# Kernel optimization log

Measured on AMD Instinct MI355X. Metric: run time of the kernel, lower is better.

Reference implementation:

```python
import jax, jax.numpy as jnp
import numpy as np

B, L, CIN, DLOI, NPTS0, NPTS1, H = 2, 5000, 256, 128, 32, 8, 256
HALF = DLOI // 2
EPS = 1e-5


def _bn_params(k, c):
    k1, k2, k3, k4 = jax.random.split(k, 4)
    gamma = 1.0 + 0.1 * jax.random.normal(k1, (c,), jnp.float32)
    beta = 0.1 * jax.random.normal(k2, (c,), jnp.float32)
    mean = 0.1 * jax.random.normal(k3, (c,), jnp.float32)
    var = 0.5 + jax.random.uniform(k4, (c,), jnp.float32)
    return jnp.stack([gamma, beta, mean, var])  # [4, c]


def setup_inputs():
    key = jax.random.key(0)
    ks = jax.random.split(key, 12)
    feature = jax.random.normal(ks[0], (B, CIN, H, H), jnp.float32)
    lines = jax.random.uniform(ks[1], (B, L, 2, 2), jnp.float32, minval=0.0, maxval=255.0)
    w_fc1 = 0.05 * jax.random.normal(ks[2], (DLOI, CIN), jnp.float32)
    b_fc1 = jnp.zeros((DLOI,), jnp.float32)
    bn1 = _bn_params(ks[3], DLOI)
    c1_w = 0.1 * jax.random.normal(ks[4], (HALF, DLOI), jnp.float32)
    c1_b = jnp.zeros((HALF,), jnp.float32)
    bn2 = _bn_params(ks[5], HALF)
    c2_w = 0.1 * jax.random.normal(ks[6], (HALF, HALF, 3), jnp.float32)
    c2_b = jnp.zeros((HALF,), jnp.float32)
    bn3 = _bn_params(ks[7], HALF)
    c3_w = 0.1 * jax.random.normal(ks[8], (DLOI, HALF), jnp.float32)
    c3_b = jnp.zeros((DLOI,), jnp.float32)
    w_fc2 = 0.03 * jax.random.normal(ks[9], (4, DLOI * NPTS1), jnp.float32)
    b_fc2 = jnp.zeros((4,), jnp.float32)
    return {"feature": feature, "lines": lines, "w_fc1": w_fc1, "b_fc1": b_fc1,
            "bn1": bn1, "c1_w": c1_w, "c1_b": c1_b, "bn2": bn2, "c2_w": c2_w,
            "c2_b": c2_b, "bn3": bn3, "c3_w": c3_w, "c3_b": c3_b,
            "w_fc2": w_fc2, "b_fc2": b_fc2}


def _bn(v, p):
    # v: [N, C, P], p: [4, C] = gamma, beta, running_mean, running_var (eval mode)
    scale = (p[0] * jax.lax.rsqrt(p[3] + EPS))[None, :, None]
    shift = p[1][None, :, None]
    return (v - p[2][None, :, None]) * scale + shift


def _forward(feature, lines, w_fc1, b_fc1, bn1, c1_w, c1_b, bn2, c2_w, c2_b,
             bn3, c3_w, c3_b, w_fc2, b_fc2):
    # fc1: 1x1 conv over backbone feature -> [B, DLOI, H, H]
    x = jnp.einsum('bchw,oc->bohw', feature, w_fc1) + b_fc1[None, :, None, None]

    # sample NPTS0 points along each line: p = p0*lam + p1*(1-lam) - 0.5
    lam = jnp.linspace(0.0, 1.0, NPTS0, dtype=jnp.float32)[:, None]  # [NPTS0, 1]
    p = lines[:, :, 0:1, :] * lam + lines[:, :, 1:2, :] * (1.0 - lam) - 0.5  # [B,L,NPTS0,2]
    px, py = p[..., 0], p[..., 1]
    px0 = jnp.clip(jnp.floor(px), 0.0, H - 1.0)
    py0 = jnp.clip(jnp.floor(py), 0.0, H - 1.0)
    px1 = jnp.clip(px0 + 1.0, 0.0, H - 1.0)
    py1 = jnp.clip(py0 + 1.0, 0.0, H - 1.0)
    i0, j0 = px0.astype(jnp.int32), py0.astype(jnp.int32)
    i1, j1 = px1.astype(jnp.int32), py1.astype(jnp.int32)
    w00 = (px1 - px) * (py1 - py)
    w10 = (px - px0) * (py1 - py)
    w01 = (px1 - px) * (py - py0)
    w11 = (px - px0) * (py - py0)

    def gather_one(feat, i0b, j0b, i1b, j1b, a, b, c, d):
        # feat [C,H,W]; indices/weights [L, NPTS0] -> [C, L, NPTS0]
        return (feat[:, i0b, j0b] * a + feat[:, i1b, j0b] * b
                + feat[:, i0b, j1b] * c + feat[:, i1b, j1b] * d)

    xp = jax.vmap(gather_one)(x, i0, j0, i1, j1, w00, w10, w01, w11)  # [B,C,L,NPTS0]
    xp = xp.transpose(0, 2, 1, 3).reshape(B * L, DLOI, NPTS0)

    # MaxPool1d(kernel=4, stride=4): NPTS0 -> NPTS1
    xp = xp.reshape(B * L, DLOI, NPTS1, NPTS0 // NPTS1).max(-1)

    # Bottleneck1D (eval-mode BN): x + op(x)
    h = jax.nn.relu(_bn(xp, bn1))
    h = jnp.einsum('ncp,oc->nop', h, c1_w) + c1_b[None, :, None]
    h = jax.nn.relu(_bn(h, bn2))
    h = jax.lax.conv_general_dilated(h, c2_w, window_strides=(1,), padding=((1, 1),),
                                     dimension_numbers=('NCH', 'OIH', 'NCH')) + c2_b[None, :, None]
    h = jax.nn.relu(_bn(h, bn3))
    h = jnp.einsum('ncp,oc->nop', h, c3_w) + c3_b[None, :, None]
    y = xp + h

    # fc2: ReLU + Linear(DLOI*NPTS1 -> 4), then softmax scores
    flat = y.reshape(B * L, DLOI * NPTS1)
    logits = jax.nn.relu(flat) @ w_fc2.T + b_fc2
    s = jax.nn.softmax(logits, axis=-1)
    return s


def reference(feature, lines, w_fc1, b_fc1, bn1, c1_w, c1_b, bn2, c2_w, c2_b,
              bn3, c3_w, c3_b, w_fc2, b_fc2):
    return _forward(feature, lines, w_fc1, b_fc1, bn1, c1_w, c1_b, bn2, c2_w,
                    c2_b, bn3, c3_w, c3_b, w_fc2, b_fc2)
```

## Files before the change

### kernel.cpp

```cpp
#include <hip/hip_runtime.h>
#include <math.h>
#include <stdint.h>

#define HH 256
#define HW 65536
#define CIN 256
#define DLOI 128
#define NLINES 10000
#define LPB 5000

typedef _Float16 h2v  __attribute__((ext_vector_type(2)));
typedef _Float16 f16x8 __attribute__((ext_vector_type(8)));
typedef float    f32x4 __attribute__((ext_vector_type(4)));

__device__ __forceinline__ h2v u2h(unsigned int u) { return __builtin_bit_cast(h2v, u); }
__device__ __forceinline__ unsigned int h2u(h2v h) { return __builtin_bit_cast(unsigned int, h); }

__device__ __forceinline__ float fdot2(h2v a, unsigned int w, float c) {
#if __has_builtin(__builtin_amdgcn_fdot2)
    return __builtin_amdgcn_fdot2(a, u2h(w), c, false);
#else
    h2v b = u2h(w);
    return c + (float)a[0] * (float)b[0] + (float)a[1] * (float)b[1];
#endif
}

__device__ __forceinline__ h2v relu2(h2v a) {
    h2v z = (h2v)(_Float16)0.f;
#if __has_builtin(__builtin_elementwise_max)
    return __builtin_elementwise_max(a, z);
#else
    h2v r; r[0] = a[0] > z[0] ? a[0] : z[0]; r[1] = a[1] > z[1] ? a[1] : z[1]; return r;
#endif
}
__device__ __forceinline__ h2v hmax2v(h2v a, h2v b) {
#if __has_builtin(__builtin_elementwise_max)
    return __builtin_elementwise_max(a, b);
#else
    h2v r; r[0] = a[0] > b[0] ? a[0] : b[0]; r[1] = a[1] > b[1] ? a[1] : b[1]; return r;
#endif
}

__global__ __launch_bounds__(256) void prep_small(
    const float* __restrict__ w_fc1, const float* __restrict__ c1w,
    const float* __restrict__ c2w,  const float* __restrict__ c3w,
    const float* __restrict__ wfc2, const float* __restrict__ bn1,
    const float* __restrict__ bn2,  const float* __restrict__ bn3,
    _Float16* __restrict__ wf16, unsigned int* __restrict__ c1w16,
    unsigned int* __restrict__ c2w16, unsigned int* __restrict__ c3w16,
    unsigned int* __restrict__ wfc2p, unsigned int* __restrict__ bn_pk)
{
    int i = blockIdx.x * 256 + threadIdx.x;
    if (i < 32768) { wf16[i] = (_Float16)w_fc1[i]; return; }
    i -= 32768;
    if (i < 4096) {
        int c2 = i >> 6, o = i & 63;
        h2v v = { (_Float16)c1w[o * 128 + 2 * c2], (_Float16)c1w[o * 128 + 2 * c2 + 1] };
        c1w16[c2 * 64 + o] = h2u(v); return;
    }
    i -= 4096;
    if (i < 6144) {
        int o = i & 63, rem = i >> 6; int tap = rem % 3, i2 = rem / 3;
        h2v v = { (_Float16)c2w[(o * 64 + 2 * i2) * 3 + tap],
                  (_Float16)c2w[(o * 64 + 2 * i2 + 1) * 3 + tap] };
        c2w16[(i2 * 3 + tap) * 64 + o] = h2u(v); return;
    }
    i -= 6144;
    if (i < 4096) {
        int o = i & 127, i2 = i >> 7;
        h2v v = { (_Float16)c3w[o * 64 + 2 * i2], (_Float16)c3w[o * 64 + 2 * i2 + 1] };
        c3w16[i2 * 128 + o] = h2u(v); return;
    }
    i -= 4096;
    if (i < 2048) {
        int c2 = i & 63, p = (i >> 6) & 7, j = i >> 9;
        h2v v = { (_Float16)wfc2[j * 1024 + (2 * c2) * 8 + p],
                  (_Float16)wfc2[j * 1024 + (2 * c2 + 1) * 8 + p] };
        wfc2p[(j * 8 + p) * 64 + c2] = h2u(v); return;
    }
    i -= 2048;
    if (i < 128) {
        const float* bn; int C, base, hcount;
        if (i < 64)      { bn = bn1; C = 128; base = 0;   hcount = 64; }
        else if (i < 96) { bn = bn2; C = 64;  base = 128; hcount = 32; i -= 64; }
        else             { bn = bn3; C = 64;  base = 192; hcount = 32; i -= 96; }
        int c0 = 2 * i, c1 = 2 * i + 1;
        float s0 = bn[c0] * rsqrtf(bn[3 * C + c0] + 1e-5f);
        float s1 = bn[c1] * rsqrtf(bn[3 * C + c1] + 1e-5f);
        float h0 = bn[C + c0] - bn[2 * C + c0] * s0;
        float h1 = bn[C + c1] - bn[2 * C + c1] * s1;
        h2v sv = { (_Float16)s0, (_Float16)s1 };
        h2v hv = { (_Float16)h0, (_Float16)h1 };
        bn_pk[base + i] = h2u(sv);
        bn_pk[base + hcount + i] = h2u(hv);
    }
}

__global__ __launch_bounds__(256, 4) void fc1_fused(
    const float* __restrict__ feat,
    const _Float16* __restrict__ W,
    const float* __restrict__ bias,
    unsigned int* __restrict__ X)
{
    __shared__ float Tf[32 * 132];
    __shared__ _Float16 Wl[128 * 40];
    const int t = threadIdx.x;
    const int lane = t & 63, wave = t >> 6;
    const int wm = wave & 1, wn = wave >> 1;
    const int pix0g = blockIdx.x << 7;
    const int b = blockIdx.x >> 9;
    const int pix0l = pix0g & 65535;
    const float* fbase = feat + (size_t)b * (256u * 65536u) + pix0l;

    f32x4 acc[4][4];
#pragma unroll
    for (int a = 0; a < 4; a++)
#pragma unroll
        for (int c = 0; c < 4; c++) acc[a][c] = (f32x4)0.f;

    for (int ks = 0; ks < 8; ks++) {
        const int k0 = ks * 32;
        __syncthreads();
#pragma unroll
        for (int r = 0; r < 4; r++) {
            int idx = t + r * 256;
            int c = idx >> 5, p4 = idx & 31;
            float4 v = *(const float4*)(fbase + (size_t)(k0 + c) * 65536 + p4 * 4);
            *(float4*)&Tf[c * 132 + p4 * 4] = v;
        }
#pragma unroll
        for (int r = 0; r < 2; r++) {
            int idx = t + r * 256;
            int row = idx >> 2, ko = (idx & 3) * 8;
            *(uint4*)&Wl[row * 40 + ko] = *(const uint4*)(W + row * 256 + k0 + ko);
        }
        __syncthreads();
        f16x8 af[4], bf[4];
#pragma unroll
        for (int mt = 0; mt < 4; mt++)
            af[mt] = *(const f16x8*)&Wl[(wm * 64 + mt * 16 + (lane & 15)) * 40 + (lane >> 4) * 8];
#pragma unroll
        for (int nt = 0; nt < 4; nt++) {
            int q = wn * 64 + nt * 16 + (lane & 15);
            int cb = (lane >> 4) * 8;
            f16x8 v;
#pragma unroll
            for (int j = 0; j < 8; j++) v[j] = (_Float16)Tf[(cb + j) * 132 + q];
            bf[nt] = v;
        }
#pragma unroll
        for (int mt = 0; mt < 4; mt++)
#pragma unroll
            for (int nt = 0; nt < 4; nt++)
                acc[mt][nt] = __builtin_amdgcn_mfma_f32_16x16x32_f16(af[mt], bf[nt], acc[mt][nt], 0, 0, 0);
    }
#pragma unroll
    for (int mt = 0; mt < 4; mt++) {
        int o = wm * 64 + mt * 16 + (lane >> 4) * 4;
        float4 b4 = *(const float4*)(bias + o);
#pragma unroll
        for (int nt = 0; nt < 4; nt++) {
            int pix = pix0g + wn * 64 + nt * 16 + (lane & 15);
            f32x4 a = acc[mt][nt];
            h2v lo = { (_Float16)(a[0] + b4.x), (_Float16)(a[1] + b4.y) };
            h2v hi = { (_Float16)(a[2] + b4.z), (_Float16)(a[3] + b4.w) };
            uint2 v = { h2u(lo), h2u(hi) };
            *(uint2*)(X + (size_t)pix * 64 + (o >> 1)) = v;
        }
    }
}

__global__ __launch_bounds__(256, 4) void line_v3(
    const unsigned int* __restrict__ X,
    const float* __restrict__ lines,
    const unsigned int* __restrict__ c1w16, const float* __restrict__ c1b,
    const unsigned int* __restrict__ c2w16, const float* __restrict__ c2b,
    const unsigned int* __restrict__ c3w16, const float* __restrict__ c3b,
    const unsigned int* __restrict__ wfc2p, const float* __restrict__ bfc2,
    const unsigned int* __restrict__ bn_pk,
    float* __restrict__ out)
{
    __shared__ int geoB[256];
    __shared__ unsigned int geoWA[256], geoWB[256];
    __shared__ h2v xp[64 * 65];
    __shared__ h2v hb[32 * 65];
    __shared__ h2v ap[32 * 73];
    __shared__ float red[128];

    const int t = threadIdx.x;
    const int n0 = blockIdx.x * 8;
    const int col = t & 63;
    const int og = t >> 6;

    {
        int l = t >> 5, k = t & 31;
        int n = n0 + l;
        float4 ln = *(const float4*)(lines + n * 4);
        float lam = (float)k / 31.0f;
        float px = ln.x * lam + ln.z * (1.f - lam) - 0.5f;
        float py = ln.y * lam + ln.w * (1.f - lam) - 0.5f;
        float px0 = fminf(fmaxf(floorf(px), 0.f), 255.f);
        float py0 = fminf(fmaxf(floorf(py), 0.f), 255.f);
        float dx = px - px0, dy = py - py0;
        float ex = 1.f - dx, ey = 1.f - dy;
        h2v wA = { (_Float16)(ex * ey), (_Float16)(dx * ey) };
        h2v wB = { (_Float16)(ex * dy), (_Float16)(dx * dy) };
        int b = (n >= LPB) ? 1 : 0;
        int pixflat = (b << 16) + ((int)px0 << 8) + (int)py0;
        geoB[t] = pixflat << 6;
        geoWA[t] = h2u(wA); geoWB[t] = h2u(wB);
    }
    __syncthreads();

    {
        const int c8 = t & 15;
        const int sub = t >> 4;
        const int line = sub >> 1;
        const int gbase = (sub & 1) * 4;
        const uint4* xq = (const uint4*)X;
#pragma unroll
        for (int lg = 0; lg < 4; lg++) {
            int g = gbase + lg;
            int ptb = line * 32 + g * 4;
            h2v m0, m1, m2, m3;
#pragma unroll
            for (int s = 0; s < 4; s++) {
                int pt = ptb + s;
                int base4 = (geoB[pt] >> 2) + c8;
                h2v wA = u2h(geoWA[pt]), wB = u2h(geoWB[pt]);
                uint4 q00 = xq[base4];
                uint4 q10 = xq[base4 + 4096];
                uint4 q01 = xq[base4 + 16];
                uint4 q11 = xq[base4 + 4112];
                h2v w00 = { wA[0], wA[0] }, w10 = { wA[1], wA[1] };
                h2v w01 = { wB[0], wB[0] }, w11 = { wB[1], wB[1] };
                h2v v0 = u2h(q00.x) * w00 + u2h(q10.x) * w10 + u2h(q01.x) * w01 + u2h(q11.x) * w11;
                h2v v1 = u2h(q00.y) * w00 + u2h(q10.y) * w10 + u2h(q01.y) * w01 + u2h(q11.y) * w11;
                h2v v2 = u2h(q00.z) * w00 + u2h(q10.z) * w10 + u2h(q01.z) * w01 + u2h(q11.z) * w11;
                h2v v3 = u2h(q00.w) * w00 + u2h(q10.w) * w10 + u2h(q01.w) * w01 + u2h(q11.w) * w11;
                if (s == 0) { m0 = v0; m1 = v1; m2 = v2; m3 = v3; }
                else { m0 = hmax2v(m0, v0); m1 = hmax2v(m1, v1);
                       m2 = hmax2v(m2, v2); m3 = hmax2v(m3, v3); }
            }
            int colw = line * 8 + g;
            xp[(c8 * 4 + 0) * 65 + colw] = m0;
            xp[(c8 * 4 + 1) * 65 + colw] = m1;
            xp[(c8 * 4 + 2) * 65 + colw] = m2;
            xp[(c8 * 4 + 3) * 65 + colw] = m3;
        }
    }
    __syncthreads();

    {
        const int obU = __builtin_amdgcn_readfirstlane(og * 16);
        float acc[16];
#pragma unroll
        for (int i = 0; i < 16; i++) acc[i] = c1b[obU + i];
#pragma unroll 8
        for (int c2 = 0; c2 < 64; c2++) {
            h2v sc = u2h(bn_pk[c2]), sh = u2h(bn_pk[64 + c2]);
            h2v av = relu2(xp[c2 * 65 + col] * sc + sh);
            unsigned int wv[16];
#pragma unroll
            for (int q = 0; q < 4; q++)
                *(uint4*)&wv[q * 4] = *(const uint4*)(c1w16 + c2 * 64 + obU + q * 4);
#pragma unroll
            for (int i = 0; i < 16; i++) acc[i] = fdot2(av, wv[i], acc[i]);
        }
#pragma unroll
        for (int j = 0; j < 8; j++) {
            h2v v = { (_Float16)acc[2 * j], (_Float16)acc[2 * j + 1] };
            hb[(obU / 2 + j) * 65 + col] = v;
        }
    }
    __syncthreads();

    {
        int c2 = t >> 3, l = t & 7;
        h2v sc = u2h(bn_pk[128 + c2]), sh = u2h(bn_pk[160 + c2]);
        h2v z = (h2v)(_Float16)0.f;
        ap[c2 * 73 + l * 9] = z;
#pragma unroll
        for (int p = 0; p < 8; p++)
            ap[c2 * 73 + l * 9 + 1 + p] = relu2(hb[c2 * 65 + l * 8 + p] * sc + sh);
        if (l == 7) ap[c2 * 73 + 72] = z;
    }
    __syncthreads();

    {
        const int obU = __builtin_amdgcn_readfirstlane(og * 16);
        const int l = col >> 3, p = col & 7;
        const int pos0 = l * 9 + p;
        float acc[16];
#pragma unroll
        for (int i = 0; i < 16; i++) acc[i] = c2b[obU + i];
#pragma unroll 2
        for (int i2 = 0; i2 < 32; i2++) {
            h2v a0 = ap[i2 * 73 + pos0];
            h2v a1 = ap[i2 * 73 + pos0 + 1];
            h2v a2 = ap[i2 * 73 + pos0 + 2];
            unsigned int wv[48];
#pragma unroll
            for (int tap = 0; tap < 3; tap++)
#pragma unroll
                for (int q = 0; q < 4; q++)
                    *(uint4*)&wv[tap * 16 + q * 4] =
                        *(const uint4*)(c2w16 + (i2 * 3 + tap) * 64 + obU + q * 4);
#pragma unroll
            for (int i = 0; i < 16; i++) {
                acc[i] = fdot2(a0, wv[i], acc[i]);
                acc[i] = fdot2(a1, wv[16 + i], acc[i]);
                acc[i] = fdot2(a2, wv[32 + i], acc[i]);
            }
        }
#pragma unroll
        for (int j = 0; j < 8; j++) {
            h2v v = { (_Float16)acc[2 * j], (_Float16)acc[2 * j + 1] };
            hb[(obU / 2 + j) * 65 + col] = v;
        }
    }
    __syncthreads();

#pragma unroll
    for (int r = 0; r < 8; r++) {
        int idx = t + 256 * r;
        int c2 = idx >> 6, cl = idx & 63;
        h2v sc = u2h(bn_pk[192 + c2]), sh = u2h(bn_pk[224 + c2]);
        ap[c2 * 64 + cl] = relu2(hb[c2 * 65 + cl] * sc + sh);
    }
    __syncthreads();

    {
        const int obU = __builtin_amdgcn_readfirstlane(og * 32);
        float acc[32];
#pragma unroll
        for (int i = 0; i < 32; i++) acc[i] = c3b[obU + i];
#pragma unroll 2
        for (int i2 = 0; i2 < 32; i2++) {
            h2v av = ap[i2 * 64 + col];
            unsigned int wv[32];
#pragma unroll
            for (int q = 0; q < 8; q++)
                *(uint4*)&wv[q * 4] = *(const uint4*)(c3w16 + i2 * 128 + obU + q * 4);
#pragma unroll
            for (int i = 0; i < 32; i++) acc[i] = fdot2(av, wv[i], acc[i]);
        }
        const int p = col & 7, l = col >> 3;
        h2v yv[16];
#pragma unroll
        for (int j = 0; j < 16; j++) {
            h2v hv = { (_Float16)acc[2 * j], (_Float16)acc[2 * j + 1] };
            yv[j] = relu2(xp[(obU / 2 + j) * 65 + col] + hv);
        }
        float aj[4] = { 0.f, 0.f, 0.f, 0.f };
#pragma unroll
        for (int j = 0; j < 4; j++) {
            unsigned int wv2[16];
#pragma unroll
            for (int q = 0; q < 4; q++)
                *(uint4*)&wv2[q * 4] = *(const uint4*)(wfc2p + (j * 8 + p) * 64 + obU / 2 + q * 4);
#pragma unroll
            for (int j16 = 0; j16 < 16; j16++) aj[j] = fdot2(yv[j16], wv2[j16], aj[j]);
        }
#pragma unroll
        for (int off = 4; off > 0; off >>= 1) {
#pragma unroll
            for (int j = 0; j < 4; j++) aj[j] += __shfl_down(aj[j], off, 8);
        }
        if ((t & 7) == 0) {
#pragma unroll
            for (int j = 0; j < 4; j++) red[og * 32 + l * 4 + j] = aj[j];
        }
    }
    __syncthreads();

    if (t < 8) {
        float lg[4];
#pragma unroll
        for (int j = 0; j < 4; j++)
            lg[j] = bfc2[j] + red[t * 4 + j] + red[32 + t * 4 + j]
                  + red[64 + t * 4 + j] + red[96 + t * 4 + j];
        float mx = fmaxf(fmaxf(lg[0], lg[1]), fmaxf(lg[2], lg[3]));
        float e0 = expf(lg[0] - mx), e1 = expf(lg[1] - mx);
        float e2 = expf(lg[2] - mx), e3 = expf(lg[3] - mx);
        float s = 1.f / (e0 + e1 + e2 + e3);
        float4 r = { e0 * s, e1 * s, e2 * s, e3 * s };
        *(float4*)(out + (size_t)(n0 + t) * 4) = r;
    }
}

extern "C" void kernel_launch(void* const* d_in, const int* in_sizes, int n_in,
                              void* d_out, int out_size, void* d_ws, size_t ws_size,
                              hipStream_t stream) {
    const float* feature = (const float*)d_in[0];
    const float* lines   = (const float*)d_in[1];
    const float* w_fc1   = (const float*)d_in[2];
    const float* b_fc1   = (const float*)d_in[3];
    const float* bn1     = (const float*)d_in[4];
    const float* c1_w    = (const float*)d_in[5];
    const float* c1_b    = (const float*)d_in[6];
    const float* bn2     = (const float*)d_in[7];
    const float* c2_w    = (const float*)d_in[8];
    const float* c2_b    = (const float*)d_in[9];
    const float* bn3     = (const float*)d_in[10];
    const float* c3_w    = (const float*)d_in[11];
    const float* c3_b    = (const float*)d_in[12];
    const float* w_fc2   = (const float*)d_in[13];
    const float* b_fc2   = (const float*)d_in[14];
    float* out = (float*)d_out;

    char* ws = (char*)d_ws;
    unsigned int* X     = (unsigned int*)ws;
    _Float16*     wf16  = (_Float16*)(ws + 33554432);
    unsigned int* c1w16 = (unsigned int*)(ws + 33619968);
    unsigned int* c2w16 = (unsigned int*)(ws + 33636352);
    unsigned int* c3w16 = (unsigned int*)(ws + 33660928);
    unsigned int* wfc2p = (unsigned int*)(ws + 33677312);
    unsigned int* bn_pk = (unsigned int*)(ws + 33685504);

    prep_small<<<193, 256, 0, stream>>>(w_fc1, c1_w, c2_w, c3_w, w_fc2, bn1, bn2, bn3,
                                        wf16, c1w16, c2w16, c3w16, wfc2p, bn_pk);
    fc1_fused<<<1024, 256, 0, stream>>>(feature, wf16, b_fc1, X);
    line_v3<<<1250, 256, 0, stream>>>(X, lines, c1w16, c1_b, c2w16, c2_b,
                                      c3w16, c3_b, wfc2p, b_fc2, bn_pk, out);
}
```

Baseline: 318.9 us.

## Move bottleneck convolutions in line kernel from fdot2 to MFMA

Rewrites the three per-line bottleneck layers (1x1, 3-tap, 1x1 convs) to use 16x16x32 f16 MFMA instructions instead of scalar packed fdot2 loops. Weights are re-laid out row-major in f16 for MFMA A-fragments, and activations are stored in LDS in a column-major padded layout. BN1 and ReLU are fused into the sampling/maxpool stage, and the residual add is applied in the MFMA epilogue. The aim is to cut the VALU-bound dot-product work. In exchange there are more LDS layout constraints, an extra buffer, and padding-zero handling for the conv taps.

```diff
diff --git a/kernel.cpp b/kernel.cpp
--- a/kernel.cpp
+++ b/kernel.cpp
@@ -3,10 +3,6 @@
 #include <stdint.h>
 
 #define HH 256
-#define HW 65536
-#define CIN 256
-#define DLOI 128
-#define NLINES 10000
 #define LPB 5000
 
 typedef _Float16 h2v  __attribute__((ext_vector_type(2)));
@@ -46,32 +42,26 @@
     const float* __restrict__ c2w,  const float* __restrict__ c3w,
     const float* __restrict__ wfc2, const float* __restrict__ bn1,
     const float* __restrict__ bn2,  const float* __restrict__ bn3,
-    _Float16* __restrict__ wf16, unsigned int* __restrict__ c1w16,
-    unsigned int* __restrict__ c2w16, unsigned int* __restrict__ c3w16,
+    _Float16* __restrict__ wf16, _Float16* __restrict__ w1r,
+    _Float16* __restrict__ w2r, _Float16* __restrict__ w3r,
     unsigned int* __restrict__ wfc2p, unsigned int* __restrict__ bn_pk)
 {
     int i = blockIdx.x * 256 + threadIdx.x;
     if (i < 32768) { wf16[i] = (_Float16)w_fc1[i]; return; }
     i -= 32768;
-    if (i < 4096) {
-        int c2 = i >> 6, o = i & 63;
-        h2v v = { (_Float16)c1w[o * 128 + 2 * c2], (_Float16)c1w[o * 128 + 2 * c2 + 1] };
-        c1w16[c2 * 64 + o] = h2u(v); return;
-    }
-    i -= 4096;
-    if (i < 6144) {
-        int o = i & 63, rem = i >> 6; int tap = rem % 3, i2 = rem / 3;
-        h2v v = { (_Float16)c2w[(o * 64 + 2 * i2) * 3 + tap],
-                  (_Float16)c2w[(o * 64 + 2 * i2 + 1) * 3 + tap] };
-        c2w16[(i2 * 3 + tap) * 64 + o] = h2u(v); return;
-    }
-    i -= 6144;
-    if (i < 4096) {
-        int o = i & 127, i2 = i >> 7;
-        h2v v = { (_Float16)c3w[o * 64 + 2 * i2], (_Float16)c3w[o * 64 + 2 * i2 + 1] };
-        c3w16[i2 * 128 + o] = h2u(v); return;
-    }
-    i -= 4096;
+    if (i < 8192) {
+        w1r[i] = (_Float16)c1w[i]; return;
+    }
+    i -= 8192;
+    if (i < 12288) {
+        int ii = i & 63, o = (i >> 6) & 63, tap = i >> 12;
+        w2r[i] = (_Float16)c2w[(o * 64 + ii) * 3 + tap]; return;
+    }
+    i -= 12288;
+    if (i < 8192) {
+        w3r[i] = (_Float16)c3w[i]; return;
+    }
+    i -= 8192;
     if (i < 2048) {
         int c2 = i & 63, p = (i >> 6) & 7, j = i >> 9;
         h2v v = { (_Float16)wfc2[j * 1024 + (2 * c2) * 8 + p],
@@ -170,27 +160,29 @@
     }
 }
 
-__global__ __launch_bounds__(256, 4) void line_v3(
+__global__ __launch_bounds__(256, 4) void line_v4(
     const unsigned int* __restrict__ X,
     const float* __restrict__ lines,
-    const unsigned int* __restrict__ c1w16, const float* __restrict__ c1b,
-    const unsigned int* __restrict__ c2w16, const float* __restrict__ c2b,
-    const unsigned int* __restrict__ c3w16, const float* __restrict__ c3b,
+    const _Float16* __restrict__ w1r, const float* __restrict__ c1b,
+    const _Float16* __restrict__ w2r, const float* __restrict__ c2b,
+    const _Float16* __restrict__ w3r, const float* __restrict__ c3b,
     const unsigned int* __restrict__ wfc2p, const float* __restrict__ bfc2,
     const unsigned int* __restrict__ bn_pk,
     float* __restrict__ out)
 {
     __shared__ int geoB[256];
     __shared__ unsigned int geoWA[256], geoWB[256];
-    __shared__ h2v xp[64 * 65];
-    __shared__ h2v hb[32 * 65];
-    __shared__ h2v ap[32 * 73];
+    __shared__ unsigned int xp[64 * 68];
+    __shared__ unsigned int abuf[64 * 68];
     __shared__ float red[128];
 
     const int t = threadIdx.x;
     const int n0 = blockIdx.x * 8;
-    const int col = t & 63;
-    const int og = t >> 6;
+    const int lane = t & 63;
+    const int w = t >> 6;
+    const int l15 = lane & 15;
+    const int kg = lane >> 4;
+    const int ko8 = kg * 8;
 
     {
         int l = t >> 5, k = t & 31;
@@ -218,6 +210,8 @@
         const int line = sub >> 1;
         const int gbase = (sub & 1) * 4;
         const uint4* xq = (const uint4*)X;
+        uint4 s1 = *(const uint4*)(bn_pk + c8 * 4);
+        uint4 h1 = *(const uint4*)(bn_pk + 64 + c8 * 4);
 #pragma unroll
         for (int lg = 0; lg < 4; lg++) {
             int g = gbase + lg;
@@ -243,122 +237,154 @@
                        m2 = hmax2v(m2, v2); m3 = hmax2v(m3, v3); }
             }
             int colw = line * 8 + g;
-            xp[(c8 * 4 + 0) * 65 + colw] = m0;
-            xp[(c8 * 4 + 1) * 65 + colw] = m1;
-            xp[(c8 * 4 + 2) * 65 + colw] = m2;
-            xp[(c8 * 4 + 3) * 65 + colw] = m3;
-        }
-    }
-    __syncthreads();
-
-    {
-        const int obU = __builtin_amdgcn_readfirstlane(og * 16);
-        float acc[16];
-#pragma unroll
-        for (int i = 0; i < 16; i++) acc[i] = c1b[obU + i];
-#pragma unroll 8
-        for (int c2 = 0; c2 < 64; c2++) {
-            h2v sc = u2h(bn_pk[c2]), sh = u2h(bn_pk[64 + c2]);
-            h2v av = relu2(xp[c2 * 65 + col] * sc + sh);
-            unsigned int wv[16];
-#pragma unroll
-            for (int q = 0; q < 4; q++)
-                *(uint4*)&wv[q * 4] = *(const uint4*)(c1w16 + c2 * 64 + obU + q * 4);
-#pragma unroll
-            for (int i = 0; i < 16; i++) acc[i] = fdot2(av, wv[i], acc[i]);
-        }
-#pragma unroll
-        for (int j = 0; j < 8; j++) {
-            h2v v = { (_Float16)acc[2 * j], (_Float16)acc[2 * j + 1] };
-            hb[(obU / 2 + j) * 65 + col] = v;
-        }
-    }
-    __syncthreads();
-
-    {
-        int c2 = t >> 3, l = t & 7;
-        h2v sc = u2h(bn_pk[128 + c2]), sh = u2h(bn_pk[160 + c2]);
-        h2v z = (h2v)(_Float16)0.f;
-        ap[c2 * 73 + l * 9] = z;
-#pragma unroll
-        for (int p = 0; p < 8; p++)
-            ap[c2 * 73 + l * 9 + 1 + p] = relu2(hb[c2 * 65 + l * 8 + p] * sc + sh);
-        if (l == 7) ap[c2 * 73 + 72] = z;
-    }
-    __syncthreads();
-
-    {
-        const int obU = __builtin_amdgcn_readfirstlane(og * 16);
-        const int l = col >> 3, p = col & 7;
-        const int pos0 = l * 9 + p;
-        float acc[16];
-#pragma unroll
-        for (int i = 0; i < 16; i++) acc[i] = c2b[obU + i];
-#pragma unroll 2
-        for (int i2 = 0; i2 < 32; i2++) {
-            h2v a0 = ap[i2 * 73 + pos0];
-            h2v a1 = ap[i2 * 73 + pos0 + 1];
-            h2v a2 = ap[i2 * 73 + pos0 + 2];
-            unsigned int wv[48];
-#pragma unroll
-            for (int tap = 0; tap < 3; tap++)
-#pragma unroll
-                for (int q = 0; q < 4; q++)
-                    *(uint4*)&wv[tap * 16 + q * 4] =
-                        *(const uint4*)(c2w16 + (i2 * 3 + tap) * 64 + obU + q * 4);
-#pragma unroll
-            for (int i = 0; i < 16; i++) {
-                acc[i] = fdot2(a0, wv[i], acc[i]);
-                acc[i] = fdot2(a1, wv[16 + i], acc[i]);
-                acc[i] = fdot2(a2, wv[32 + i], acc[i]);
+            uint4 raw = { h2u(m0), h2u(m1), h2u(m2), h2u(m3) };
+            *(uint4*)&xp[colw * 68 + c8 * 4] = raw;
+            h2v r0 = relu2(m0 * u2h(s1.x) + u2h(h1.x));
+            h2v r1 = relu2(m1 * u2h(s1.y) + u2h(h1.y));
+            h2v r2 = relu2(m2 * u2h(s1.z) + u2h(h1.z));
+            h2v r3 = relu2(m3 * u2h(s1.w) + u2h(h1.w));
+            uint4 act = { h2u(r0), h2u(r1), h2u(r2), h2u(r3) };
+            *(uint4*)&abuf[colw * 68 + c8 * 4] = act;
+        }
+    }
+    __syncthreads();
+
+    f32x4 acc1[4];
+#pragma unroll
+    for (int nt = 0; nt < 4; nt++) acc1[nt] = (f32x4)0.f;
+    {
+        const int o = w * 16 + l15;
+        f16x8 af[4];
+#pragma unroll
+        for (int kt = 0; kt < 4; kt++)
+            af[kt] = *(const f16x8*)(w1r + o * 128 + kt * 32 + ko8);
+#pragma unroll
+        for (int nt = 0; nt < 4; nt++) {
+            const int colb = nt * 16 + l15;
+#pragma unroll
+            for (int kt = 0; kt < 4; kt++) {
+                f16x8 bf = *(const f16x8*)&abuf[colb * 68 + kt * 16 + kg * 4];
+                acc1[nt] = __builtin_amdgcn_mfma_f32_16x16x32_f16(af[kt], bf, acc1[nt], 0, 0, 0);
             }
         }
-#pragma unroll
-        for (int j = 0; j < 8; j++) {
-            h2v v = { (_Float16)acc[2 * j], (_Float16)acc[2 * j + 1] };
-            hb[(obU / 2 + j) * 65 + col] = v;
-        }
-    }
-    __syncthreads();
-
-#pragma unroll
-    for (int r = 0; r < 8; r++) {
-        int idx = t + 256 * r;
-        int c2 = idx >> 6, cl = idx & 63;
-        h2v sc = u2h(bn_pk[192 + c2]), sh = u2h(bn_pk[224 + c2]);
-        ap[c2 * 64 + cl] = relu2(hb[c2 * 65 + cl] * sc + sh);
-    }
-    __syncthreads();
-
-    {
-        const int obU = __builtin_amdgcn_readfirstlane(og * 32);
-        float acc[32];
-#pragma unroll
-        for (int i = 0; i < 32; i++) acc[i] = c3b[obU + i];
-#pragma unroll 2
-        for (int i2 = 0; i2 < 32; i2++) {
-            h2v av = ap[i2 * 64 + col];
-            unsigned int wv[32];
-#pragma unroll
-            for (int q = 0; q < 8; q++)
-                *(uint4*)&wv[q * 4] = *(const uint4*)(c3w16 + i2 * 128 + obU + q * 4);
-#pragma unroll
-            for (int i = 0; i < 32; i++) acc[i] = fdot2(av, wv[i], acc[i]);
-        }
+    }
+    __syncthreads();
+
+    {
+        float4 b1 = *(const float4*)(c1b + w * 16 + kg * 4);
+        const int o2 = w * 8 + kg * 2;
+        h2v sA = u2h(bn_pk[128 + o2]), sB = u2h(bn_pk[128 + o2 + 1]);
+        h2v hA = u2h(bn_pk[160 + o2]), hB = u2h(bn_pk[160 + o2 + 1]);
+#pragma unroll
+        for (int nt = 0; nt < 4; nt++) {
+            const int col = nt * 16 + l15;
+            const int colp = (col >> 3) * 10 + 1 + (col & 7);
+            h2v v0 = { (_Float16)(acc1[nt][0] + b1.x), (_Float16)(acc1[nt][1] + b1.y) };
+            h2v v1 = { (_Float16)(acc1[nt][2] + b1.z), (_Float16)(acc1[nt][3] + b1.w) };
+            v0 = relu2(v0 * sA + hA);
+            v1 = relu2(v1 * sB + hB);
+            uint2 u = { h2u(v0), h2u(v1) };
+            *(uint2*)&abuf[colp * 36 + o2] = u;
+        }
+#pragma unroll
+        for (int e = 0; e < 2; e++) {
+            int idx = t * 2 + e;
+            int pc = idx >> 5, i2 = idx & 31;
+            int pl = pc >> 1, side = pc & 1;
+            abuf[(pl * 10 + side * 9) * 36 + i2] = 0;
+        }
+    }
+    __syncthreads();
+
+    f32x4 acc2[4];
+#pragma unroll
+    for (int nt = 0; nt < 4; nt++) acc2[nt] = (f32x4)0.f;
+    {
+        const int o = w * 16 + l15;
+        const int colp0 = (l15 >> 3) * 10 + 1 + (l15 & 7);
+#pragma unroll
+        for (int tap = 0; tap < 3; tap++) {
+            f16x8 wa0 = *(const f16x8*)(w2r + (tap * 64 + o) * 64 + ko8);
+            f16x8 wa1 = *(const f16x8*)(w2r + (tap * 64 + o) * 64 + 32 + ko8);
+#pragma unroll
+            for (int nt = 0; nt < 4; nt++) {
+                const int cp = colp0 + nt * 20 + tap - 1;
+                f16x8 b0 = *(const f16x8*)&abuf[cp * 36 + kg * 4];
+                f16x8 b1 = *(const f16x8*)&abuf[cp * 36 + 16 + kg * 4];
+                acc2[nt] = __builtin_amdgcn_mfma_f32_16x16x32_f16(wa0, b0, acc2[nt], 0, 0, 0);
+                acc2[nt] = __builtin_amdgcn_mfma_f32_16x16x32_f16(wa1, b1, acc2[nt], 0, 0, 0);
+            }
+        }
+    }
+    __syncthreads();
+
+    {
+        float4 b2 = *(const float4*)(c2b + w * 16 + kg * 4);
+        const int o2 = w * 8 + kg * 2;
+        h2v sA = u2h(bn_pk[192 + o2]), sB = u2h(bn_pk[192 + o2 + 1]);
+        h2v hA = u2h(bn_pk[224 + o2]), hB = u2h(bn_pk[224 + o2 + 1]);
+#pragma unroll
+        for (int nt = 0; nt < 4; nt++) {
+            const int col = nt * 16 + l15;
+            h2v v0 = { (_Float16)(acc2[nt][0] + b2.x), (_Float16)(acc2[nt][1] + b2.y) };
+            h2v v1 = { (_Float16)(acc2[nt][2] + b2.z), (_Float16)(acc2[nt][3] + b2.w) };
+            v0 = relu2(v0 * sA + hA);
+            v1 = relu2(v1 * sB + hB);
+            uint2 u = { h2u(v0), h2u(v1) };
+            *(uint2*)&abuf[col * 36 + o2] = u;
+        }
+    }
+    __syncthreads();
+
+    {
+#pragma unroll
+        for (int mi = 0; mi < 2; mi++) {
+            const int om = (2 * w + mi) * 16 + l15;
+            f16x8 af0 = *(const f16x8*)(w3r + om * 64 + ko8);
+            f16x8 af1 = *(const f16x8*)(w3r + om * 64 + 32 + ko8);
+            f32x4 acc3[4];
+#pragma unroll
+            for (int nt = 0; nt < 4; nt++) acc3[nt] = (f32x4)0.f;
+#pragma unroll
+            for (int nt = 0; nt < 4; nt++) {
+                const int col = nt * 16 + l15;
+                f16x8 b0 = *(const f16x8*)&abuf[col * 36 + kg * 4];
+                f16x8 b1 = *(const f16x8*)&abuf[col * 36 + 16 + kg * 4];
+                acc3[nt] = __builtin_amdgcn_mfma_f32_16x16x32_f16(af0, b0, acc3[nt], 0, 0, 0);
+                acc3[nt] = __builtin_amdgcn_mfma_f32_16x16x32_f16(af1, b1, acc3[nt], 0, 0, 0);
+            }
+            float4 b3 = *(const float4*)(c3b + (2 * w + mi) * 16 + kg * 4);
+            const int o2 = (2 * w + mi) * 8 + kg * 2;
+#pragma unroll
+            for (int nt = 0; nt < 4; nt++) {
+                const int col = nt * 16 + l15;
+                uint2 xv = *(const uint2*)&xp[col * 68 + o2];
+                h2v y0 = { (_Float16)(acc3[nt][0] + b3.x), (_Float16)(acc3[nt][1] + b3.y) };
+                h2v y1 = { (_Float16)(acc3[nt][2] + b3.z), (_Float16)(acc3[nt][3] + b3.w) };
+                y0 = relu2(u2h(xv.x) + y0);
+                y1 = relu2(u2h(xv.y) + y1);
+                uint2 u = { h2u(y0), h2u(y1) };
+                *(uint2*)&xp[col * 68 + o2] = u;
+            }
+        }
+    }
+    __syncthreads();
+
+    {
+        const int og = w;
+        const int col = t & 63;
+        const int obH = __builtin_amdgcn_readfirstlane(og * 16);
         const int p = col & 7, l = col >> 3;
         h2v yv[16];
 #pragma unroll
-        for (int j = 0; j < 16; j++) {
-            h2v hv = { (_Float16)acc[2 * j], (_Float16)acc[2 * j + 1] };
-            yv[j] = relu2(xp[(obU / 2 + j) * 65 + col] + hv);
-        }
+        for (int j = 0; j < 16; j++) yv[j] = u2h(xp[col * 68 + obH + j]);
         float aj[4] = { 0.f, 0.f, 0.f, 0.f };
 #pragma unroll
         for (int j = 0; j < 4; j++) {
             unsigned int wv2[16];
 #pragma unroll
             for (int q = 0; q < 4; q++)
-                *(uint4*)&wv2[q * 4] = *(const uint4*)(wfc2p + (j * 8 + p) * 64 + obU / 2 + q * 4);
+                *(uint4*)&wv2[q * 4] = *(const uint4*)(wfc2p + (j * 8 + p) * 64 + obH + q * 4);
 #pragma unroll
             for (int j16 = 0; j16 < 16; j16++) aj[j] = fdot2(yv[j16], wv2[j16], aj[j]);
         }
@@ -412,15 +438,15 @@
     char* ws = (char*)d_ws;
     unsigned int* X     = (unsigned int*)ws;
     _Float16*     wf16  = (_Float16*)(ws + 33554432);
-    unsigned int* c1w16 = (unsigned int*)(ws + 33619968);
-    unsigned int* c2w16 = (unsigned int*)(ws + 33636352);
-    unsigned int* c3w16 = (unsigned int*)(ws + 33660928);
+    _Float16*     w1r   = (_Float16*)(ws + 33619968);
+    _Float16*     w2r   = (_Float16*)(ws + 33636352);
+    _Float16*     w3r   = (_Float16*)(ws + 33660928);
     unsigned int* wfc2p = (unsigned int*)(ws + 33677312);
     unsigned int* bn_pk = (unsigned int*)(ws + 33685504);
 
-    prep_small<<<193, 256, 0, stream>>>(w_fc1, c1_w, c2_w, c3_w, w_fc2, bn1, bn2, bn3,
-                                        wf16, c1w16, c2w16, c3w16, wfc2p, bn_pk);
+    prep_small<<<249, 256, 0, stream>>>(w_fc1, c1_w, c2_w, c3_w, w_fc2, bn1, bn2, bn3,
+                                        wf16, w1r, w2r, w3r, wfc2p, bn_pk);
     fc1_fused<<<1024, 256, 0, stream>>>(feature, wf16, b_fc1, X);
-    line_v3<<<1250, 256, 0, stream>>>(X, lines, c1w16, c1_b, c2w16, c2_b,
-                                      c3w16, c3_b, wfc2p, b_fc2, bn_pk, out);
-}
+    line_v4<<<1250, 256, 0, stream>>>(X, lines, w1r, c1_b, w2r, c2_b,
+                                      w3r, c3_b, wfc2p, b_fc2, bn_pk, out);
+}
```

New measurement: 267.4 us, median of 2. -16.2%, faster.
